# Optimization experiments

Hardware: AMD Instinct MI355X
Metric: run time of the kernel (lower is better)

## Reference

```python
import jax, jax.numpy as jnp
import numpy as np

N_NODES = 51200
N_EDGES = 819200
N_GRAPHS = 256


def _p(k, shape, scale=0.05):
    return jax.random.normal(k, shape, jnp.float32) * scale


def setup_inputs() -> dict:
    key = jax.random.key(0)
    ks = jax.random.split(key, 32)
    inp = {
        "x": jax.random.normal(ks[0], (N_NODES, 128), jnp.float32),
        "src": jax.random.randint(ks[1], (N_EDGES,), 0, N_NODES, jnp.int32),
        "dst": jax.random.randint(ks[2], (N_EDGES,), 0, N_NODES, jnp.int32),
        "graph_ids": jnp.sort(jax.random.randint(ks[3], (N_NODES,), 0, N_GRAPHS, jnp.int32)),
        "edge_weight": jax.random.uniform(ks[4], (N_EDGES,), jnp.float32),
        "conv1_w": _p(ks[5], (96, 128, 3)), "conv1_b": _p(ks[6], (96,)),
        "conv2_w": _p(ks[7], (96, 128, 3)), "conv2_b": _p(ks[8], (96,)),
        "conv3_w": _p(ks[9], (96, 128, 3)), "conv3_b": _p(ks[10], (96,)),
        "W11": _p(ks[11], (96, 54)), "b11": _p(ks[12], (54,)),
        "W12": _p(ks[13], (96, 54)), "b12": _p(ks[14], (54,)),
        "W13": _p(ks[15], (96, 54)), "b13": _p(ks[16], (54,)),
        "W2": _p(ks[17], (54, 25)), "b2": _p(ks[18], (25,)),
        "W3": _p(ks[19], (25, 13)), "b3": _p(ks[20], (13,)),
        "W4": _p(ks[21], (25, 11)), "b4": _p(ks[22], (11,)),
        "Wc1": _p(ks[23], (49, 27)), "bc1": _p(ks[24], (27,)),
        "Wc2": _p(ks[25], (27, 5)), "bc2": _p(ks[26], (5,)),
    }
    return inp


def _conv1d(x_ncw, k_oiw, b, dilation, pad):
    # x: [1,128,N], k: [96,128,3] -> [1,96,N]
    y = jax.lax.conv_general_dilated(
        x_ncw, k_oiw, window_strides=(1,), padding=[(pad, pad)],
        rhs_dilation=(dilation,), dimension_numbers=("NCH", "OIH", "NCH"))
    return y + b[None, :, None]


def reference(x, src, dst, graph_ids, edge_weight,
              conv1_w, conv1_b, conv2_w, conv2_b, conv3_w, conv3_b,
              W11, b11, W12, b12, W13, b13, W2, b2, W3, b3, W4, b4,
              Wc1, bc1, Wc2, bc2):
    relu = jax.nn.relu
    h0 = x.T[None]  # [1,128,N] — conv over the batched node sequence, as in torch
    c1 = _conv1d(h0, conv1_w, conv1_b, 1, 1)[0].T  # [N,96]
    c2 = _conv1d(h0, conv2_w, conv2_b, 2, 2)[0].T
    c3 = _conv1d(h0, conv3_w, conv3_b, 3, 3)[0].T
    h01 = relu(c1) + c2
    h02 = relu(c2) + c3
    h03 = relu(c3) + c1

    def gconv(h, W, b):
        # DGL GraphConv norm='none', in>out: transform first, then weighted scatter-sum
        hw = h @ W                              # [N,out]
        msg = hw[src] * edge_weight[:, None]    # [E,out]
        return jax.ops.segment_sum(msg, dst, num_segments=N_NODES) + b

    ac_h1 = relu(gconv(h01, W11, b11)) + relu(gconv(h02, W12, b12)) + relu(gconv(h03, W13, b13))
    ac_h2 = relu(gconv(ac_h1, W2, b2))
    ac_h3 = relu(gconv(ac_h2, W3, b3))
    ac_h4 = relu(gconv(ac_h2, W4, b4))

    seg = lambda v: jax.ops.segment_sum(v, graph_ids, num_segments=N_GRAPHS)
    hg = jnp.concatenate([seg(ac_h2), seg(ac_h3), seg(ac_h4)], axis=1)  # [G,49]
    return (hg @ Wc1 + bc1) @ Wc2 + bc2  # [G,5]
```

## Files before the change

kernel.cpp:

```cpp
#include <hip/hip_runtime.h>
#include <hip/hip_bf16.h>

#define N_NODES 51200
#define N_EDGES 819200
#define N_GRAPHS 256

typedef __attribute__((ext_vector_type(8))) short short8;
typedef __attribute__((ext_vector_type(4))) float f32x4;

__device__ __forceinline__ ushort f2bf(float f) {
    uint u = __builtin_bit_cast(uint, f);
    u += 0x7FFFu + ((u >> 16) & 1u);
    return (ushort)(u >> 16);
}
__device__ __forceinline__ float bf2f(ushort h) {
    uint u = ((uint)h) << 16;
    return __builtin_bit_cast(float, u);
}

__global__ __launch_bounds__(256) void k_init(
    const float* __restrict__ w1, const float* __restrict__ w2,
    const float* __restrict__ w3,
    const float* __restrict__ W11, const float* __restrict__ W12,
    const float* __restrict__ W13,
    const float* __restrict__ b11, const float* __restrict__ b12,
    const float* __restrict__ b13,
    ushort* __restrict__ Wtc, ushort* __restrict__ Wp1,
    float* __restrict__ bias_cat,
    float* __restrict__ hg, int* __restrict__ cnt) {
    int idx = blockIdx.x * 256 + threadIdx.x;
    if (idx < N_GRAPHS * 49) hg[idx] = 0.f;
    if (idx < N_NODES) cnt[idx] = 0;
    if (idx < 176)
        bias_cat[idx] = (idx < 54) ? b11[idx] : (idx < 108) ? b12[idx - 54]
                      : (idx < 162) ? b13[idx - 108] : 0.f;
    if (idx < 3 * 12 * 96 * 32) {
        int kl = idx & 31;
        int o  = (idx >> 5) % 96;
        int s  = (idx >> 5) / 96 % 12;
        int k  = idx / (32 * 96 * 12);
        int kk = s * 32 + kl;
        int t = kk >> 7, i = kk & 127;
        const float* w = (k == 0) ? w1 : (k == 1) ? w2 : w3;
        Wtc[idx] = f2bf(w[(o * 128 + i) * 3 + t]);
    }
    if (idx < 3 * 3 * 64 * 32) {
        int kl = idx & 31;
        int o  = (idx >> 5) % 64;
        int s2 = (idx >> 5) / 64 % 3;
        int k  = idx / (32 * 64 * 3);
        int kk2 = s2 * 32 + kl;
        const float* W = (k == 0) ? W11 : (k == 1) ? W12 : W13;
        Wp1[idx] = (o < 54) ? f2bf(W[kk2 * 54 + o]) : (ushort)0;
    }
}

#define RNG 6400
#define ECHUNK 4096
#define DEG_MAX 64
#define BN 64
#define XS_LD 136
#define HS_LD 104

__global__ __launch_bounds__(256, 4) void k_convscat(
    const float* __restrict__ x,
    const ushort* __restrict__ Wtc, const ushort* __restrict__ Wp1g,
    const float* __restrict__ b1, const float* __restrict__ b2,
    const float* __restrict__ b3, ushort* __restrict__ hw_cat,
    const int* __restrict__ src, const int* __restrict__ dst,
    const float* __restrict__ ew,
    int* __restrict__ cnt, uint* __restrict__ s_pack) {
    __shared__ ushort xs[70 * XS_LD];
    __shared__ ushort wl[9216];

    const int tid = threadIdx.x;
    const int gid = blockIdx.x >> 3;
    const int sub = blockIdx.x & 7;

    if (gid % 3 != 2) {
        int c = (gid / 3) * 2 + (gid % 3);
        int lo = sub * RNG, hi = lo + RNG;
        int base = c * ECHUNK + tid;
#pragma unroll
        for (int i = 0; i < ECHUNK / 256; ++i) {
            int e = base + i * 256;
            int d = dst[e];
            int sv = src[e];
            float wv = ew[e];
            if (d >= lo && d < hi) {
                int pos = atomicAdd(&cnt[d], 1);
                if (pos < DEG_MAX)
                    s_pack[(d << 6) + pos] = ((uint)f2bf(wv) << 16) | (uint)sv;
            }
        }
        return;
    }

    const int tile = (gid / 3) * 8 + sub;
    const int n0   = tile * BN;
    ushort* wp   = wl;
    ushort* hswb = xs;

    for (int idx = tid; idx < 70 * 32; idx += 256) {
        int row = idx >> 5, c4 = (idx & 31) << 2;
        int node = n0 - 3 + row;
        float4 v = make_float4(0.f, 0.f, 0.f, 0.f);
        if (node >= 0 && node < N_NODES)
            v = *reinterpret_cast<const float4*>(x + (size_t)node * 128 + c4);
        ushort* p = &xs[row * XS_LD + c4];
        p[0] = f2bf(v.x); p[1] = f2bf(v.y); p[2] = f2bf(v.z); p[3] = f2bf(v.w);
    }

    const int lane = tid & 63;
    const int wave = tid >> 6;
    const int r16  = lane & 15;
    const int b8   = (lane >> 4) * 8;

    f32x4 acc[3][6];
#pragma unroll
    for (int k = 0; k < 3; ++k)
#pragma unroll
        for (int ot = 0; ot < 6; ++ot) acc[k][ot] = (f32x4)0.f;

    ushort4 wreg[9];
#pragma unroll
    for (int i = 0; i < 9; ++i)
        wreg[i] = *reinterpret_cast<const ushort4*>(Wtc + (i * 256 + tid) * 4);

#pragma unroll
    for (int kq = 0; kq < 12; ++kq) {
        const int k = kq >> 2;
        const int q = kq & 3;
        __syncthreads();
#pragma unroll
        for (int i = 0; i < 9; ++i)
            *reinterpret_cast<ushort4*>(wl + (i * 256 + tid) * 4) = wreg[i];
        __syncthreads();
        if (kq < 11) {
            const ushort* nw = Wtc + (size_t)(kq + 1) * 9216;
#pragma unroll
            for (int i = 0; i < 9; ++i)
                wreg[i] = *reinterpret_cast<const ushort4*>(nw + (i * 256 + tid) * 4);
        }
        const int dk = k + 1;
#pragma unroll
        for (int sp = 0; sp < 3; ++sp) {
            const int s     = q * 3 + sp;
            const int cbase = (s * 32) & 127;
            const int t     = (s * 32) >> 7;
            const int roff  = (t - 1) * dk + 3;
            short8 a = *reinterpret_cast<const short8*>(
                &xs[(wave * 16 + r16 + roff) * XS_LD + cbase + b8]);
#pragma unroll
            for (int ot = 0; ot < 6; ++ot) {
                short8 b = *reinterpret_cast<const short8*>(
                    &wl[(sp * 96 + ot * 16 + r16) * 32 + b8]);
                acc[k][ot] = __builtin_amdgcn_mfma_f32_16x16x32_bf16(a, b, acc[k][ot], 0, 0, 0);
            }
        }
    }

#pragma unroll
    for (int ot = 0; ot < 6; ++ot) {
        int o = ot * 16 + r16;
        float bb1 = b1[o], bb2 = b2[o], bb3 = b3[o];
#pragma unroll
        for (int r = 0; r < 4; ++r) {
            float C1 = acc[0][ot][r] + bb1;
            float C2 = acc[1][ot][r] + bb2;
            float C3 = acc[2][ot][r] + bb3;
            acc[0][ot][r] = fmaxf(C1, 0.f) + C2;
            acc[1][ot][r] = fmaxf(C2, 0.f) + C3;
            acc[2][ot][r] = fmaxf(C3, 0.f) + C1;
        }
    }

    ushort* hs = hswb + wave * (16 * HS_LD);
#pragma unroll
    for (int k = 0; k < 3; ++k) {
        __syncthreads();
#pragma unroll
        for (int i = 0; i < 6; ++i)
            *reinterpret_cast<ushort4*>(wp + (i * 256 + tid) * 4) =
                *reinterpret_cast<const ushort4*>(Wp1g + k * 6144 + (i * 256 + tid) * 4);
#pragma unroll
        for (int ot = 0; ot < 6; ++ot)
#pragma unroll
            for (int r = 0; r < 4; ++r)
                hs[((lane >> 4) * 4 + r) * HS_LD + ot * 16 + r16] = f2bf(acc[k][ot][r]);
        __syncthreads();
        f32x4 acc2[4];
#pragma unroll
        for (int ot2 = 0; ot2 < 4; ++ot2) acc2[ot2] = (f32x4)0.f;
#pragma unroll
        for (int s2 = 0; s2 < 3; ++s2) {
            short8 a = *reinterpret_cast<const short8*>(&hs[r16 * HS_LD + s2 * 32 + b8]);
#pragma unroll
            for (int ot2 = 0; ot2 < 4; ++ot2) {
                short8 b = *reinterpret_cast<const short8*>(
                    &wp[(s2 * 64 + ot2 * 16 + r16) * 32 + b8]);
                acc2[ot2] = __builtin_amdgcn_mfma_f32_16x16x32_bf16(a, b, acc2[ot2], 0, 0, 0);
            }
        }
#pragma unroll
        for (int ot2 = 0; ot2 < 4; ++ot2) {
            int co = ot2 * 16 + r16;
            if (co < 54) {
#pragma unroll
                for (int r = 0; r < 4; ++r) {
                    int node = n0 + wave * 16 + (lane >> 4) * 4 + r;
                    hw_cat[(size_t)node * 176 + k * 54 + co] = f2bf(acc2[ot2][r]);
                }
            }
        }
    }
    for (int idx = tid; idx < 64 * 14; idx += 256) {
        int r = idx / 14, c = 162 + (idx - r * 14);
        hw_cat[(size_t)(n0 + r) * 176 + c] = 0;
    }
}

__global__ __launch_bounds__(256) void k_agg1(
    const ushort* __restrict__ hw, const int* __restrict__ cnt,
    const uint* __restrict__ pk, const float* __restrict__ bias_cat,
    const float* __restrict__ W2, ushort* __restrict__ hw2) {
    __shared__ float stage[4][176];
    __shared__ float w2s[54 * 25];
    int tid = threadIdx.x;
    for (int i = tid; i < 54 * 25; i += 256) w2s[i] = W2[i];
    int lane = tid & 63, wave = tid >> 6;
    int n = blockIdx.x * 4 + wave;
    const bool act = lane < 44;
    const int col = lane * 4;
    int e0 = n << 6;
    int e1 = e0 + __builtin_amdgcn_readfirstlane(cnt[n]);
    float a0 = 0.f, a1 = 0.f, a2 = 0.f, a3 = 0.f;
    int e = e0;
    if (e + 7 < e1) {
        uint m[8];
#pragma unroll
        for (int u = 0; u < 8; ++u) m[u] = pk[e + u];
        for (;;) {
            bool more = (e + 15 < e1);
            uint mn[8];
            if (more) {
#pragma unroll
                for (int u = 0; u < 8; ++u) mn[u] = pk[e + 8 + u];
            }
            if (act) {
#pragma unroll
                for (int u = 0; u < 8; ++u) {
                    float w = bf2f((ushort)(m[u] >> 16));
                    ushort4 v = *reinterpret_cast<const ushort4*>(
                        hw + (size_t)(m[u] & 0xFFFFu) * 176 + col);
                    a0 += w * bf2f(v.x); a1 += w * bf2f(v.y);
                    a2 += w * bf2f(v.z); a3 += w * bf2f(v.w);
                }
            }
            e += 8;
            if (!more) break;
#pragma unroll
            for (int u = 0; u < 8; ++u) m[u] = mn[u];
        }
    }
    if (e + 3 < e1) {
        uint m[4];
#pragma unroll
        for (int u = 0; u < 4; ++u) m[u] = pk[e + u];
        if (act) {
#pragma unroll
            for (int u = 0; u < 4; ++u) {
                float w = bf2f((ushort)(m[u] >> 16));
                ushort4 v = *reinterpret_cast<const ushort4*>(
                    hw + (size_t)(m[u] & 0xFFFFu) * 176 + col);
                a0 += w * bf2f(v.x); a1 += w * bf2f(v.y);
                a2 += w * bf2f(v.z); a3 += w * bf2f(v.w);
            }
        }
        e += 4;
    }
    for (; e < e1; ++e) {
        uint m = pk[e];
        if (act) {
            float w = bf2f((ushort)(m >> 16));
            ushort4 v = *reinterpret_cast<const ushort4*>(
                hw + (size_t)(m & 0xFFFFu) * 176 + col);
            a0 += w * bf2f(v.x); a1 += w * bf2f(v.y);
            a2 += w * bf2f(v.z); a3 += w * bf2f(v.w);
        }
    }
    if (act) {
        stage[wave][col + 0] = fmaxf(a0 + bias_cat[col + 0], 0.f);
        stage[wave][col + 1] = fmaxf(a1 + bias_cat[col + 1], 0.f);
        stage[wave][col + 2] = fmaxf(a2 + bias_cat[col + 2], 0.f);
        stage[wave][col + 3] = fmaxf(a3 + bias_cat[col + 3], 0.f);
    }
    __syncthreads();
    if (lane < 54)
        stage[wave][lane] = stage[wave][lane] + stage[wave][lane + 54] +
                            stage[wave][lane + 108];
    if (lane < 25) {
        float acc = 0.f;
#pragma unroll
        for (int i = 0; i < 54; ++i) acc += stage[wave][i] * w2s[i * 25 + lane];
        hw2[(size_t)n * 28 + lane] = f2bf(acc);
    }
}

__global__ __launch_bounds__(256) void k_agg2(
    const ushort* __restrict__ hw2, const int* __restrict__ cnt,
    const uint* __restrict__ pk,
    const float* __restrict__ b2, const float* __restrict__ W3,
    const float* __restrict__ W4, const int* __restrict__ gids,
    ushort* __restrict__ hw34, float* __restrict__ hg) {
    __shared__ float w34s[25 * 24];
    __shared__ float vst[8][26];
    __shared__ int sgid[8];
    int tid = threadIdx.x;
    for (int i = tid; i < 25 * 24; i += 256) {
        int ii = i / 24, j = i - ii * 24;
        w34s[i] = (j < 13) ? W3[ii * 13 + j] : W4[ii * 11 + (j - 13)];
    }
    int lane = tid & 63, wave = tid >> 6;
    int half = lane >> 5, jj = lane & 31;
    int n0b = blockIdx.x * 8;
    int nl = wave * 2 + half;
    int n = n0b + nl;
    int e0 = n << 6;
    int e1 = e0 + cnt[n];
    float acc = 0.f;
    int e = e0;
    for (; e + 7 < e1; e += 8) {
        uint m[8];
#pragma unroll
        for (int u = 0; u < 8; ++u) m[u] = pk[e + u];
        if (jj < 25) {
#pragma unroll
            for (int u = 0; u < 8; ++u)
                acc += bf2f((ushort)(m[u] >> 16)) *
                       bf2f(hw2[(size_t)(m[u] & 0xFFFFu) * 28 + jj]);
        }
    }
    if (e + 3 < e1) {
        uint m[4];
#pragma unroll
        for (int u = 0; u < 4; ++u) m[u] = pk[e + u];
        if (jj < 25) {
#pragma unroll
            for (int u = 0; u < 4; ++u)
                acc += bf2f((ushort)(m[u] >> 16)) *
                       bf2f(hw2[(size_t)(m[u] & 0xFFFFu) * 28 + jj]);
        }
        e += 4;
    }
    for (; e < e1; ++e) {
        uint m = pk[e];
        if (jj < 25) acc += bf2f((ushort)(m >> 16)) *
                            bf2f(hw2[(size_t)(m & 0xFFFFu) * 28 + jj]);
    }
    if (jj < 25) vst[nl][jj] = fmaxf(acc + b2[jj], 0.f);
    if (jj == 0) sgid[nl] = gids[n];
    __syncthreads();
    if (tid < 25) {
        float run = vst[0][tid];
        int g = sgid[0];
        for (int nn = 1; nn < 8; ++nn) {
            if (sgid[nn] == g) run += vst[nn][tid];
            else { atomicAdd(&hg[g * 49 + tid], run); run = vst[nn][tid]; g = sgid[nn]; }
        }
        atomicAdd(&hg[g * 49 + tid], run);
    }
    if (tid < 192) {
        int node = tid / 24, j = tid - node * 24;
        float a = 0.f;
#pragma unroll
        for (int i = 0; i < 25; ++i) a += vst[node][i] * w34s[i * 24 + j];
        hw34[(size_t)(n0b + node) * 24 + j] = f2bf(a);
    }
}

__global__ __launch_bounds__(256) void k_agg34(
    const ushort* __restrict__ hw34, const int* __restrict__ cnt,
    const uint* __restrict__ pk,
    const float* __restrict__ b3, const float* __restrict__ b4,
    const int* __restrict__ gids, float* __restrict__ hg) {
    __shared__ float vst[8][25];
    __shared__ int sgid[8];
    int tid = threadIdx.x;
    int lane = tid & 63, wave = tid >> 6;
    int half = lane >> 5, jj = lane & 31;
    int nl = wave * 2 + half;
    int n = blockIdx.x * 8 + nl;
    int e0 = n << 6;
    int e1 = e0 + cnt[n];
    float acc = 0.f;
    int e = e0;
    for (; e + 7 < e1; e += 8) {
        uint m[8];
#pragma unroll
        for (int u = 0; u < 8; ++u) m[u] = pk[e + u];
        if (jj < 24) {
#pragma unroll
            for (int u = 0; u < 8; ++u)
                acc += bf2f((ushort)(m[u] >> 16)) *
                       bf2f(hw34[(size_t)(m[u] & 0xFFFFu) * 24 + jj]);
        }
    }
    if (e + 3 < e1) {
        uint m[4];
#pragma unroll
        for (int u = 0; u < 4; ++u) m[u] = pk[e + u];
        if (jj < 24) {
#pragma unroll
            for (int u = 0; u < 4; ++u)
                acc += bf2f((ushort)(m[u] >> 16)) *
                       bf2f(hw34[(size_t)(m[u] & 0xFFFFu) * 24 + jj]);
        }
        e += 4;
    }
    for (; e < e1; ++e) {
        uint m = pk[e];
        if (jj < 24) acc += bf2f((ushort)(m >> 16)) *
                            bf2f(hw34[(size_t)(m & 0xFFFFu) * 24 + jj]);
    }
    if (jj < 24) {
        float v = (jj < 13) ? fmaxf(acc + b3[jj], 0.f)
                            : fmaxf(acc + b4[jj - 13], 0.f);
        vst[nl][jj] = v;
    }
    if (jj == 0) sgid[nl] = gids[n];
    __syncthreads();
    if (tid < 24) {
        float run = vst[0][tid];
        int g = sgid[0];
        for (int nn = 1; nn < 8; ++nn) {
            if (sgid[nn] == g) run += vst[nn][tid];
            else { atomicAdd(&hg[g * 49 + 25 + tid], run); run = vst[nn][tid]; g = sgid[nn]; }
        }
        atomicAdd(&hg[g * 49 + 25 + tid], run);
    }
}

__global__ __launch_bounds__(256) void k_final(
    const float* __restrict__ hg, const float* __restrict__ Wc1,
    const float* __restrict__ bc1, const float* __restrict__ Wc2,
    const float* __restrict__ bc2, float* __restrict__ out) {
    int g = blockIdx.x * blockDim.x + threadIdx.x;
    if (g < N_GRAPHS) {
        float t[27];
#pragma unroll
        for (int j = 0; j < 27; ++j) t[j] = bc1[j];
        for (int i = 0; i < 49; ++i) {
            float hv = hg[g * 49 + i];
#pragma unroll
            for (int j = 0; j < 27; ++j) t[j] += hv * Wc1[i * 27 + j];
        }
#pragma unroll
        for (int j2 = 0; j2 < 5; ++j2) {
            float o = bc2[j2];
#pragma unroll
            for (int i = 0; i < 27; ++i) o += t[i] * Wc2[i * 5 + j2];
            out[g * 5 + j2] = o;
        }
    }
}

extern "C" void kernel_launch(void* const* d_in, const int* in_sizes, int n_in,
                              void* d_out, int out_size, void* d_ws, size_t ws_size,
                              hipStream_t stream) {
    const float* x    = (const float*)d_in[0];
    const int*   src  = (const int*)d_in[1];
    const int*   dst  = (const int*)d_in[2];
    const int*   gids = (const int*)d_in[3];
    const float* ew   = (const float*)d_in[4];
    const float* w1 = (const float*)d_in[5],  *b1 = (const float*)d_in[6];
    const float* w2 = (const float*)d_in[7],  *b2 = (const float*)d_in[8];
    const float* w3 = (const float*)d_in[9],  *b3 = (const float*)d_in[10];
    const float* W11 = (const float*)d_in[11], *b11 = (const float*)d_in[12];
    const float* W12 = (const float*)d_in[13], *b12 = (const float*)d_in[14];
    const float* W13 = (const float*)d_in[15], *b13 = (const float*)d_in[16];
    const float* W2  = (const float*)d_in[17], *b2g = (const float*)d_in[18];
    const float* W3  = (const float*)d_in[19], *b3g = (const float*)d_in[20];
    const float* W4  = (const float*)d_in[21], *b4g = (const float*)d_in[22];
    const float* Wc1 = (const float*)d_in[23], *bc1 = (const float*)d_in[24];
    const float* Wc2 = (const float*)d_in[25], *bc2 = (const float*)d_in[26];
    float* out = (float*)d_out;

    char* ws = (char*)d_ws;
    size_t off = 0;
    auto alloc = [&](size_t bytes) {
        size_t o = off;
        off = (off + bytes + 255) & ~(size_t)255;
        return (void*)(ws + o);
    };
    int*    cnt      = (int*)alloc(N_NODES * 4);
    uint*   s_pack   = (uint*)alloc((size_t)N_NODES * DEG_MAX * 4);
    ushort* hw_cat   = (ushort*)alloc((size_t)N_NODES * 176 * 2);
    ushort* hw2      = (ushort*)alloc((size_t)N_NODES * 28 * 2);
    ushort* hw34     = (ushort*)alloc((size_t)N_NODES * 24 * 2);
    float*  hg       = (float*)alloc(N_GRAPHS * 49 * 4);
    ushort* Wtc      = (ushort*)alloc(3 * 12 * 96 * 32 * 2);
    ushort* Wp1      = (ushort*)alloc(3 * 3 * 64 * 32 * 2);
    float*  bias_cat = (float*)alloc(176 * 4);

    k_init<<<(3 * 12 * 96 * 32 + 255) / 256, 256, 0, stream>>>(
        w1, w2, w3, W11, W12, W13, b11, b12, b13, Wtc, Wp1, bias_cat, hg, cnt);
    k_convscat<<<2400, 256, 0, stream>>>(x, Wtc, Wp1, b1, b2, b3, hw_cat,
                                         src, dst, ew, cnt, s_pack);
    k_agg1<<<N_NODES / 4, 256, 0, stream>>>(hw_cat, cnt, s_pack,
                                            bias_cat, W2, hw2);
    k_agg2<<<N_NODES / 8, 256, 0, stream>>>(hw2, cnt, s_pack, b2g,
                                            W3, W4, gids, hw34, hg);
    k_agg34<<<N_NODES / 8, 256, 0, stream>>>(hw34, cnt, s_pack, b3g, b4g,
                                             gids, hg);
    k_final<<<1, 256, 0, stream>>>(hg, Wc1, bc1, Wc2, bc2, out);
}
```

Measured before the change: 195.3 us.

## Shrink conv weight staging chunks, raise occupancy, vectorize agg1 edge loads

Splits the conv weight staging into 18 smaller chunks of 6144 elements instead of 12 of 9216, shrinking the LDS weight buffer and register prefetch so that five blocks per CU can be requested instead of four. Weight copies now use 16-byte vector loads and stores. In k_agg1, the edge-list loop is rewritten to fetch packed edges as uint4 groups of 16, with a predicated tail instead of the nested 8/4/1 loops. Degree counts are clamped to DEG_MAX in all aggregation kernels, which bounds reads to the per-node slot region. The cost is more barrier rounds in the conv kernel and possible register-pressure spills at the higher occupancy target.

```diff
diff --git a/kernel.cpp b/kernel.cpp
--- a/kernel.cpp
+++ b/kernel.cpp
@@ -62,7 +62,7 @@
 #define XS_LD 136
 #define HS_LD 104
 
-__global__ __launch_bounds__(256, 4) void k_convscat(
+__global__ __launch_bounds__(256, 5) void k_convscat(
     const float* __restrict__ x,
     const ushort* __restrict__ Wtc, const ushort* __restrict__ Wp1g,
     const float* __restrict__ b1, const float* __restrict__ b2,
@@ -71,7 +71,7 @@
     const float* __restrict__ ew,
     int* __restrict__ cnt, uint* __restrict__ s_pack) {
     __shared__ ushort xs[70 * XS_LD];
-    __shared__ ushort wl[9216];
+    __shared__ ushort wl[6144];
 
     const int tid = threadIdx.x;
     const int gid = blockIdx.x >> 3;
@@ -122,30 +122,30 @@
 #pragma unroll
         for (int ot = 0; ot < 6; ++ot) acc[k][ot] = (f32x4)0.f;
 
-    ushort4 wreg[9];
-#pragma unroll
-    for (int i = 0; i < 9; ++i)
-        wreg[i] = *reinterpret_cast<const ushort4*>(Wtc + (i * 256 + tid) * 4);
-
-#pragma unroll
-    for (int kq = 0; kq < 12; ++kq) {
-        const int k = kq >> 2;
-        const int q = kq & 3;
+    short8 wreg[3];
+#pragma unroll
+    for (int i = 0; i < 3; ++i)
+        wreg[i] = *reinterpret_cast<const short8*>(Wtc + (i * 256 + tid) * 8);
+
+#pragma unroll
+    for (int ch = 0; ch < 18; ++ch) {
+        const int k  = ch / 6;
+        const int cp = ch % 6;
         __syncthreads();
 #pragma unroll
-        for (int i = 0; i < 9; ++i)
-            *reinterpret_cast<ushort4*>(wl + (i * 256 + tid) * 4) = wreg[i];
+        for (int i = 0; i < 3; ++i)
+            *reinterpret_cast<short8*>(wl + (i * 256 + tid) * 8) = wreg[i];
         __syncthreads();
-        if (kq < 11) {
-            const ushort* nw = Wtc + (size_t)(kq + 1) * 9216;
-#pragma unroll
-            for (int i = 0; i < 9; ++i)
-                wreg[i] = *reinterpret_cast<const ushort4*>(nw + (i * 256 + tid) * 4);
+        if (ch < 17) {
+            const ushort* nw = Wtc + (size_t)(ch + 1) * 6144;
+#pragma unroll
+            for (int i = 0; i < 3; ++i)
+                wreg[i] = *reinterpret_cast<const short8*>(nw + (i * 256 + tid) * 8);
         }
         const int dk = k + 1;
 #pragma unroll
-        for (int sp = 0; sp < 3; ++sp) {
-            const int s     = q * 3 + sp;
+        for (int sp = 0; sp < 2; ++sp) {
+            const int s     = cp * 2 + sp;
             const int cbase = (s * 32) & 127;
             const int t     = (s * 32) >> 7;
             const int roff  = (t - 1) * dk + 3;
@@ -180,9 +180,9 @@
     for (int k = 0; k < 3; ++k) {
         __syncthreads();
 #pragma unroll
-        for (int i = 0; i < 6; ++i)
-            *reinterpret_cast<ushort4*>(wp + (i * 256 + tid) * 4) =
-                *reinterpret_cast<const ushort4*>(Wp1g + k * 6144 + (i * 256 + tid) * 4);
+        for (int i = 0; i < 3; ++i)
+            *reinterpret_cast<short8*>(wp + (i * 256 + tid) * 8) =
+                *reinterpret_cast<const short8*>(Wp1g + k * 6144 + (i * 256 + tid) * 8);
 #pragma unroll
         for (int ot = 0; ot < 6; ++ot)
 #pragma unroll
@@ -232,63 +232,45 @@
     int n = blockIdx.x * 4 + wave;
     const bool act = lane < 44;
     const int col = lane * 4;
-    int e0 = n << 6;
-    int e1 = e0 + __builtin_amdgcn_readfirstlane(cnt[n]);
+    int deg = __builtin_amdgcn_readfirstlane(cnt[n]);
+    deg = deg > DEG_MAX ? DEG_MAX : deg;
+    const uint4* pk4 = reinterpret_cast<const uint4*>(pk + ((size_t)n << 6));
     float a0 = 0.f, a1 = 0.f, a2 = 0.f, a3 = 0.f;
-    int e = e0;
-    if (e + 7 < e1) {
-        uint m[8];
-#pragma unroll
-        for (int u = 0; u < 8; ++u) m[u] = pk[e + u];
-        for (;;) {
-            bool more = (e + 15 < e1);
-            uint mn[8];
-            if (more) {
-#pragma unroll
-                for (int u = 0; u < 8; ++u) mn[u] = pk[e + 8 + u];
+
+    auto proc = [&](uint mm) {
+        float w = bf2f((ushort)(mm >> 16));
+        ushort4 v = *reinterpret_cast<const ushort4*>(
+            hw + (size_t)(mm & 0xFFFFu) * 176 + col);
+        a0 += w * bf2f(v.x); a1 += w * bf2f(v.y);
+        a2 += w * bf2f(v.z); a3 += w * bf2f(v.w);
+    };
+
+    int e = 0;
+    for (; e + 16 <= deg; e += 16) {
+        uint4 M[4];
+#pragma unroll
+        for (int g = 0; g < 4; ++g) M[g] = pk4[(e >> 2) + g];
+        if (act) {
+#pragma unroll
+            for (int g = 0; g < 4; ++g) {
+                proc(M[g].x); proc(M[g].y); proc(M[g].z); proc(M[g].w);
             }
-            if (act) {
-#pragma unroll
-                for (int u = 0; u < 8; ++u) {
-                    float w = bf2f((ushort)(m[u] >> 16));
-                    ushort4 v = *reinterpret_cast<const ushort4*>(
-                        hw + (size_t)(m[u] & 0xFFFFu) * 176 + col);
-                    a0 += w * bf2f(v.x); a1 += w * bf2f(v.y);
-                    a2 += w * bf2f(v.z); a3 += w * bf2f(v.w);
-                }
-            }
-            e += 8;
-            if (!more) break;
-#pragma unroll
-            for (int u = 0; u < 8; ++u) m[u] = mn[u];
-        }
-    }
-    if (e + 3 < e1) {
-        uint m[4];
-#pragma unroll
-        for (int u = 0; u < 4; ++u) m[u] = pk[e + u];
-        if (act) {
-#pragma unroll
-            for (int u = 0; u < 4; ++u) {
-                float w = bf2f((ushort)(m[u] >> 16));
-                ushort4 v = *reinterpret_cast<const ushort4*>(
-                    hw + (size_t)(m[u] & 0xFFFFu) * 176 + col);
-                a0 += w * bf2f(v.x); a1 += w * bf2f(v.y);
-                a2 += w * bf2f(v.z); a3 += w * bf2f(v.w);
-            }
-        }
-        e += 4;
-    }
-    for (; e < e1; ++e) {
-        uint m = pk[e];
-        if (act) {
-            float w = bf2f((ushort)(m >> 16));
-            ushort4 v = *reinterpret_cast<const ushort4*>(
-                hw + (size_t)(m & 0xFFFFu) * 176 + col);
-            a0 += w * bf2f(v.x); a1 += w * bf2f(v.y);
-            a2 += w * bf2f(v.z); a3 += w * bf2f(v.w);
-        }
-    }
+        }
+    }
+    if (e < deg) {
+        uint4 M[4];
+#pragma unroll
+        for (int g = 0; g < 4; ++g) M[g] = pk4[(e >> 2) + g];
+        uint mm[16] = {M[0].x, M[0].y, M[0].z, M[0].w,
+                       M[1].x, M[1].y, M[1].z, M[1].w,
+                       M[2].x, M[2].y, M[2].z, M[2].w,
+                       M[3].x, M[3].y, M[3].z, M[3].w};
+        int rem = deg - e;
+#pragma unroll
+        for (int u = 0; u < 16; ++u)
+            if (u < rem && act) proc(mm[u]);
+    }
+
     if (act) {
         stage[wave][col + 0] = fmaxf(a0 + bias_cat[col + 0], 0.f);
         stage[wave][col + 1] = fmaxf(a1 + bias_cat[col + 1], 0.f);
@@ -327,7 +309,8 @@
     int nl = wave * 2 + half;
     int n = n0b + nl;
     int e0 = n << 6;
-    int e1 = e0 + cnt[n];
+    int dcg = cnt[n];
+    int e1 = e0 + (dcg > DEG_MAX ? DEG_MAX : dcg);
     float acc = 0.f;
     int e = e0;
     for (; e + 7 < e1; e += 8) {
@@ -392,7 +375,8 @@
     int nl = wave * 2 + half;
     int n = blockIdx.x * 8 + nl;
     int e0 = n << 6;
-    int e1 = e0 + cnt[n];
+    int dcg = cnt[n];
+    int e1 = e0 + (dcg > DEG_MAX ? DEG_MAX : dcg);
     float acc = 0.f;
     int e = e0;
     for (; e + 7 < e1; e += 8) {
```

After: 215.6 us. +10.4%, slower.
